# Optimization experiments

Hardware: AMD Instinct MI355X
Metric: run time of the kernel (lower is better)

## Reference

```python
import jax, jax.numpy as jnp
import numpy as np

TEMPERATURE = 0.07
EPS = 1e-07


def setup_inputs() -> dict:
    key = jax.random.key(0)
    kf, kl = jax.random.split(key)
    bsz, n_views, d = 4096, 2, 256
    feats = jax.random.normal(kf, (bsz, n_views, d), dtype=jnp.float32)
    # L2-normalize per view, as in standard SupCon pipelines
    feats = feats / jnp.linalg.norm(feats, axis=-1, keepdims=True)
    labels = jax.random.randint(kl, (bsz,), 0, 3, dtype=jnp.int64 if jax.config.jax_enable_x64 else jnp.int32)
    return {"features": feats, "labels": labels}


def reference(features, labels):
    bsz, n_views, d = features.shape
    n = bsz * n_views
    # torch.cat(torch.unbind(features, dim=1), dim=0): views stacked along batch
    contrast_feature = jnp.transpose(features, (1, 0, 2)).reshape(n, d)
    anchor_feature = contrast_feature  # contrast_mode == 'all'

    # label-equality mask with the module's 1e-7 offset, tiled over views
    mask_small = (labels[:, None] == labels[None, :]).astype(jnp.float32) + EPS
    mask = jnp.tile(mask_small, (n_views, n_views))  # [n, n]

    logits_mask = 1.0 - jnp.eye(n, dtype=jnp.float32)  # zero out self-contrast
    mask_pos = mask * logits_mask
    mask_neg = (1.0 - mask) * logits_mask

    similarity = jnp.exp(jnp.matmul(anchor_feature, contrast_feature.T) / TEMPERATURE)
    pos = jnp.sum(similarity * mask_pos, axis=1)
    neg = jnp.sum(similarity * mask_neg, axis=1)
    loss = -jnp.mean(jnp.log(pos / (pos + neg)))
    return loss
```

## Files before the change

kernel.cpp:

```cpp
#include <hip/hip_runtime.h>
#include <cstdint>

#define BSZ   4096
#define NTOT  8192
#define DIM   256
#define BT    128
#define BKE   128
#define NCB   (NTOT / BT)
#define NBLK  (NCB * (NCB + 1) / 2)
#define INV_T (1.0f/0.07f)

typedef __bf16 bf16x8 __attribute__((ext_vector_type(8)));
typedef float  f32x4  __attribute__((ext_vector_type(4)));

#define GLOAD_LDS16(gp, lp)                                                  \
  __builtin_amdgcn_global_load_lds(                                          \
      (const __attribute__((address_space(1))) void*)(gp),                   \
      (__attribute__((address_space(3))) void*)(lp), 16, 0, 0)

__device__ __forceinline__ unsigned short f2bf(float f) {
  unsigned int u = __float_as_uint(f);
  u = u + 0x7FFFu + ((u >> 16) & 1u);
  return (unsigned short)(u >> 16);
}

__global__ __launch_bounds__(256) void cvt_kernel(const float* __restrict__ F,
                                                  unsigned short* __restrict__ X,
                                                  float* __restrict__ gsum,
                                                  int* __restrict__ gcnt) {
  if (blockIdx.x == 0 && threadIdx.x == 0) { *gsum = 0.f; *gcnt = 0; }
  int t = blockIdx.x * 256 + threadIdx.x;
  int r = t >> 6;
  int k = (t & 63) << 2;
  const float4 v = *(const float4*)(F + (size_t)(r & (BSZ - 1)) * (2 * DIM)
                                      + (r >> 12) * DIM + k);
  ushort4 o = make_ushort4(f2bf(v.x), f2bf(v.y), f2bf(v.z), f2bf(v.w));
  *(ushort4*)(X + (size_t)r * DIM + k) = o;
}

__global__ __launch_bounds__(256) void supcon_kernel(
    const unsigned short* __restrict__ X, const int* __restrict__ lab,
    float* __restrict__ partTot, float* __restrict__ partEq) {
  __shared__ unsigned short lA[BT * BKE];
  __shared__ unsigned short lB[BT * BKE];

  const int tid  = threadIdx.x;
  const int lane = tid & 63;
  const int wave = tid >> 6;
  const int wr   = (wave >> 1) * 64;
  const int wc   = (wave & 1) * 64;
  const int l15  = lane & 15;
  const int quad = lane >> 4;

  const int b = blockIdx.x;
  const int c = (b & 7) * (NBLK / 8) + (b >> 3);
  int i, j;
  if (c < 1792) {
    const int spo = c >> 6;
    const int w   = c & 63;
    int g1 = 0, rem = spo;
    while (rem >= 7 - g1) { rem -= 7 - g1; ++g1; }
    const int g2 = g1 + 1 + rem;
    i = g1 * 8 + (w >> 3);
    j = g2 * 8 + (w & 7);
  } else {
    const int c2 = c - 1792;
    const int g  = c2 / 36;
    int w = c2 - g * 36;
    int a = 0;
    while (w >= 8 - a) { w -= 8 - a; ++a; }
    i = g * 8 + a;
    j = g * 8 + a + w;
  }
  const int RB = i * BT;
  const int CB = j * BT;

  int colIdx[4], colLab[4];
#pragma unroll
  for (int tc = 0; tc < 4; ++tc) {
    colIdx[tc] = CB + wc + tc * 16 + l15;
    colLab[tc] = lab[colIdx[tc] & (BSZ - 1)];
  }
  int rowLab[4][4];
#pragma unroll
  for (int tr = 0; tr < 4; ++tr)
#pragma unroll
    for (int reg = 0; reg < 4; ++reg)
      rowLab[tr][reg] = lab[(RB + wr + tr * 16 + quad * 4 + reg) & (BSZ - 1)];

  const int srow  = lane >> 4;
  const unsigned short* gA = X + (size_t)(RB + wave * 32 + srow) * DIM;
  const unsigned short* gB = X + (size_t)(CB + wave * 32 + srow) * DIM;

  f32x4 acc[4][4] = {};

  for (int kb = 0; kb < DIM; kb += BKE) {
    __syncthreads();
#pragma unroll
    for (int l = 0; l < 8; ++l) {
      const int chunk = (lane & 15) ^ ((l * 4 + srow) & 15);
      GLOAD_LDS16(gA + (size_t)(l * 4) * DIM + kb + chunk * 8,
                  lA + (wave * 32 + l * 4) * BKE);
      GLOAD_LDS16(gB + (size_t)(l * 4) * DIM + kb + chunk * 8,
                  lB + (wave * 32 + l * 4) * BKE);
    }
    __syncthreads();

#pragma unroll
    for (int sub = 0; sub < 4; ++sub) {
      bf16x8 aF[4], bF[4];
      const int slot = ((sub * 4 + quad) ^ l15) * 8;
#pragma unroll
      for (int t = 0; t < 4; ++t) {
        aF[t] = *(const bf16x8*)(lA + (wr + t * 16 + l15) * BKE + slot);
        bF[t] = *(const bf16x8*)(lB + (wc + t * 16 + l15) * BKE + slot);
      }
#pragma unroll
      for (int tr = 0; tr < 4; ++tr)
#pragma unroll
        for (int tc = 0; tc < 4; ++tc)
          acc[tr][tc] = __builtin_amdgcn_mfma_f32_16x16x32_bf16(
              aF[tr], bF[tc], acc[tr][tc], 0, 0, 0);
    }
  }

  if (i == j) {
#pragma unroll
    for (int tr = 0; tr < 4; ++tr)
#pragma unroll
      for (int tc = 0; tc < 4; ++tc)
#pragma unroll
        for (int reg = 0; reg < 4; ++reg) {
          const int row = RB + wr + tr * 16 + quad * 4 + reg;
          float e = __expf(acc[tr][tc][reg] * INV_T);
          acc[tr][tc][reg] = (colIdx[tc] == row) ? 0.f : e;
        }
  } else {
#pragma unroll
    for (int tr = 0; tr < 4; ++tr)
#pragma unroll
      for (int tc = 0; tc < 4; ++tc)
#pragma unroll
        for (int reg = 0; reg < 4; ++reg)
          acc[tr][tc][reg] = __expf(acc[tr][tc][reg] * INV_T);
  }

  __syncthreads();
  float* sbuf = (float*)lA;
#pragma unroll
  for (int tr = 0; tr < 4; ++tr) {
#pragma unroll
    for (int reg = 0; reg < 4; ++reg) {
      float tot = 0.f, eqs = 0.f;
#pragma unroll
      for (int tc = 0; tc < 4; ++tc) {
        const float e = acc[tr][tc][reg];
        tot += e;
        if (colLab[tc] == rowLab[tr][reg]) eqs += e;
      }
#pragma unroll
      for (int off = 1; off < 16; off <<= 1) {
        tot += __shfl_xor(tot, off, 64);
        eqs += __shfl_xor(eqs, off, 64);
      }
      if (l15 == 0) {
        const int rl_ = wr + tr * 16 + quad * 4 + reg;
        sbuf[(wave & 1) * 128 + rl_]       = tot;
        sbuf[256 + (wave & 1) * 128 + rl_] = eqs;
      }
    }
  }
  if (i != j) {
#pragma unroll
    for (int tc = 0; tc < 4; ++tc) {
      float tt = 0.f, te = 0.f;
#pragma unroll
      for (int tr = 0; tr < 4; ++tr)
#pragma unroll
        for (int reg = 0; reg < 4; ++reg) {
          const float e = acc[tr][tc][reg];
          tt += e;
          if (rowLab[tr][reg] == colLab[tc]) te += e;
        }
      tt += __shfl_xor(tt, 16, 64);  te += __shfl_xor(te, 16, 64);
      tt += __shfl_xor(tt, 32, 64);  te += __shfl_xor(te, 32, 64);
      if (quad == 0) {
        const int cl_ = wc + tc * 16 + l15;
        sbuf[512 + (wave >> 1) * 128 + cl_] = tt;
        sbuf[768 + (wave >> 1) * 128 + cl_] = te;
      }
    }
  }
  __syncthreads();

  if (tid < 128) {
    partTot[(size_t)j * NTOT + RB + tid] = sbuf[tid] + sbuf[128 + tid];
    partEq [(size_t)j * NTOT + RB + tid] = sbuf[256 + tid] + sbuf[384 + tid];
  } else if (i != j) {
    const int c2 = tid - 128;
    partTot[(size_t)i * NTOT + CB + c2] = sbuf[512 + c2] + sbuf[640 + c2];
    partEq [(size_t)i * NTOT + CB + c2] = sbuf[768 + c2] + sbuf[896 + c2];
  }
}

__global__ __launch_bounds__(128) void reduce_kernel(
    const float* __restrict__ partTot, const float* __restrict__ partEq,
    float* __restrict__ gsum, int* __restrict__ gcnt,
    unsigned int* __restrict__ out) {
  const int r = blockIdx.x * 128 + threadIdx.x;
  float tot = 0.f, eqs = 0.f;
#pragma unroll 8
  for (int cb = 0; cb < NCB; ++cb) {
    tot += partTot[(size_t)cb * NTOT + r];
    eqs += partEq [(size_t)cb * NTOT + r];
  }
  const float term = __logf((eqs + 1e-7f * tot) / tot);
  __shared__ float red[128];
  red[threadIdx.x] = term;
  __syncthreads();
  for (int step = 64; step > 0; step >>= 1) {
    if (threadIdx.x < step) red[threadIdx.x] += red[threadIdx.x + step];
    __syncthreads();
  }
  if (threadIdx.x == 0) {
    atomicAdd(gsum, red[0]);
    __threadfence();
    const int old = atomicAdd(gcnt, 1);
    if (old == (int)gridDim.x - 1) {
      __threadfence();
      const float total = atomicAdd(gsum, 0.0f);
      const float loss = -total / (float)NTOT;
      const unsigned short bb = f2bf(loss);
      out[0] = ((unsigned int)bb << 16) | (unsigned int)bb;
    }
  }
}

extern "C" void kernel_launch(void* const* d_in, const int* in_sizes, int n_in,
                              void* d_out, int out_size, void* d_ws, size_t ws_size,
                              hipStream_t stream) {
  (void)in_sizes; (void)n_in; (void)out_size; (void)ws_size;
  const float* feats = (const float*)d_in[0];
  const int*   labels = (const int*)d_in[1];

  char* ws = (char*)d_ws;
  unsigned short* X = (unsigned short*)ws;
  float* partTot = (float*)(ws + (size_t)NTOT * DIM * 2);
  float* partEq  = partTot + (size_t)NCB * NTOT;
  float* gsum    = partEq  + (size_t)NCB * NTOT;
  int*   gcnt    = (int*)(gsum + 1);

  cvt_kernel<<<NTOT * DIM / 4 / 256, 256, 0, stream>>>(feats, X, gsum, gcnt);
  supcon_kernel<<<NBLK, 256, 0, stream>>>(X, labels, partTot, partEq);
  reduce_kernel<<<NTOT / 128, 128, 0, stream>>>(partTot, partEq, gsum, gcnt,
                                                (unsigned int*)d_out);
}
```

Measured before the change: 115.0 us.

## Pre-swizzle features into MFMA fragment layout and load fragments directly from global

The conversion kernel now writes the bf16 features in a layout matching the MFMA 16x16x32 fragment order, so each lane's 8-element fragment is contiguous. The GEMM kernel drops the LDS staging, its swizzled global-to-LDS loads and the barriers, and reads A/B fragments straight from global/L2, with launch bounds raised to target 3 blocks per CU. This removes LDS traffic and synchronisation, but each wave now loads its own fragments and data sharing within a block depends on the cache, which raises global/L2 load traffic.

```diff
diff --git a/kernel.cpp b/kernel.cpp
--- a/kernel.cpp
+++ b/kernel.cpp
@@ -5,18 +5,12 @@
 #define NTOT  8192
 #define DIM   256
 #define BT    128
-#define BKE   128
 #define NCB   (NTOT / BT)
 #define NBLK  (NCB * (NCB + 1) / 2)
 #define INV_T (1.0f/0.07f)
 
 typedef __bf16 bf16x8 __attribute__((ext_vector_type(8)));
 typedef float  f32x4  __attribute__((ext_vector_type(4)));
-
-#define GLOAD_LDS16(gp, lp)                                                  \
-  __builtin_amdgcn_global_load_lds(                                          \
-      (const __attribute__((address_space(1))) void*)(gp),                   \
-      (__attribute__((address_space(3))) void*)(lp), 16, 0, 0)
 
 __device__ __forceinline__ unsigned short f2bf(float f) {
   unsigned int u = __float_as_uint(f);
@@ -24,25 +18,30 @@
   return (unsigned short)(u >> 16);
 }
 
+
 __global__ __launch_bounds__(256) void cvt_kernel(const float* __restrict__ F,
-                                                  unsigned short* __restrict__ X,
+                                                  unsigned short* __restrict__ Xf,
                                                   float* __restrict__ gsum,
                                                   int* __restrict__ gcnt) {
   if (blockIdx.x == 0 && threadIdx.x == 0) { *gsum = 0.f; *gcnt = 0; }
-  int t = blockIdx.x * 256 + threadIdx.x;
-  int r = t >> 6;
-  int k = (t & 63) << 2;
-  const float4 v = *(const float4*)(F + (size_t)(r & (BSZ - 1)) * (2 * DIM)
-                                      + (r >> 12) * DIM + k);
-  ushort4 o = make_ushort4(f2bf(v.x), f2bf(v.y), f2bf(v.z), f2bf(v.w));
-  *(ushort4*)(X + (size_t)r * DIM + k) = o;
-}
-
-__global__ __launch_bounds__(256) void supcon_kernel(
-    const unsigned short* __restrict__ X, const int* __restrict__ lab,
+  const int v = blockIdx.x * 256 + threadIdx.x;
+  const int T = v >> 9;
+  const int c = (v >> 4) & 31;
+  const int p = v & 15;
+  const int r = T * 16 + p;
+  const float* src = F + (size_t)(r & (BSZ - 1)) * (2 * DIM) + (r >> 12) * DIM + c * 8;
+  const float4 v0 = *(const float4*)src;
+  const float4 v1 = *(const float4*)(src + 4);
+  ushort4 o0 = make_ushort4(f2bf(v0.x), f2bf(v0.y), f2bf(v0.z), f2bf(v0.w));
+  ushort4 o1 = make_ushort4(f2bf(v1.x), f2bf(v1.y), f2bf(v1.z), f2bf(v1.w));
+  *(ushort4*)(Xf + (size_t)v * 8)     = o0;
+  *(ushort4*)(Xf + (size_t)v * 8 + 4) = o1;
+}
+
+__global__ __launch_bounds__(256, 3) void supcon_kernel(
+    const unsigned short* __restrict__ Xf, const int* __restrict__ lab,
     float* __restrict__ partTot, float* __restrict__ partEq) {
-  __shared__ unsigned short lA[BT * BKE];
-  __shared__ unsigned short lB[BT * BKE];
+  __shared__ float sbuf[1024];
 
   const int tid  = threadIdx.x;
   const int lane = tid & 63;
@@ -88,40 +87,27 @@
     for (int reg = 0; reg < 4; ++reg)
       rowLab[tr][reg] = lab[(RB + wr + tr * 16 + quad * 4 + reg) & (BSZ - 1)];
 
-  const int srow  = lane >> 4;
-  const unsigned short* gA = X + (size_t)(RB + wave * 32 + srow) * DIM;
-  const unsigned short* gB = X + (size_t)(CB + wave * 32 + srow) * DIM;
+  const int TA = (RB >> 4) + (wave >> 1) * 4;
+  const int TB = (CB >> 4) + (wave & 1) * 4;
+  const int lo = quad * 128 + l15 * 8;
 
   f32x4 acc[4][4] = {};
 
-  for (int kb = 0; kb < DIM; kb += BKE) {
-    __syncthreads();
-#pragma unroll
-    for (int l = 0; l < 8; ++l) {
-      const int chunk = (lane & 15) ^ ((l * 4 + srow) & 15);
-      GLOAD_LDS16(gA + (size_t)(l * 4) * DIM + kb + chunk * 8,
-                  lA + (wave * 32 + l * 4) * BKE);
-      GLOAD_LDS16(gB + (size_t)(l * 4) * DIM + kb + chunk * 8,
-                  lB + (wave * 32 + l * 4) * BKE);
-    }
-    __syncthreads();
-
-#pragma unroll
-    for (int sub = 0; sub < 4; ++sub) {
-      bf16x8 aF[4], bF[4];
-      const int slot = ((sub * 4 + quad) ^ l15) * 8;
-#pragma unroll
-      for (int t = 0; t < 4; ++t) {
-        aF[t] = *(const bf16x8*)(lA + (wr + t * 16 + l15) * BKE + slot);
-        bF[t] = *(const bf16x8*)(lB + (wc + t * 16 + l15) * BKE + slot);
-      }
-#pragma unroll
-      for (int tr = 0; tr < 4; ++tr)
-#pragma unroll
-        for (int tc = 0; tc < 4; ++tc)
-          acc[tr][tc] = __builtin_amdgcn_mfma_f32_16x16x32_bf16(
-              aF[tr], bF[tc], acc[tr][tc], 0, 0, 0);
-    }
+#pragma unroll
+  for (int kb = 0; kb < 8; ++kb) {
+    bf16x8 aF[4], bF[4];
+    const int ko = kb * 512 + lo;
+#pragma unroll
+    for (int t = 0; t < 4; ++t) {
+      aF[t] = *(const bf16x8*)(Xf + (size_t)(TA + t) * 4096 + ko);
+      bF[t] = *(const bf16x8*)(Xf + (size_t)(TB + t) * 4096 + ko);
+    }
+#pragma unroll
+    for (int tr = 0; tr < 4; ++tr)
+#pragma unroll
+      for (int tc = 0; tc < 4; ++tc)
+        acc[tr][tc] = __builtin_amdgcn_mfma_f32_16x16x32_bf16(
+            aF[tr], bF[tc], acc[tr][tc], 0, 0, 0);
   }
 
   if (i == j) {
@@ -145,8 +131,6 @@
           acc[tr][tc][reg] = __expf(acc[tr][tc][reg] * INV_T);
   }
 
-  __syncthreads();
-  float* sbuf = (float*)lA;
 #pragma unroll
   for (int tr = 0; tr < 4; ++tr) {
 #pragma unroll
@@ -244,14 +228,14 @@
   const int*   labels = (const int*)d_in[1];
 
   char* ws = (char*)d_ws;
-  unsigned short* X = (unsigned short*)ws;
+  unsigned short* Xf = (unsigned short*)ws;
   float* partTot = (float*)(ws + (size_t)NTOT * DIM * 2);
   float* partEq  = partTot + (size_t)NCB * NTOT;
   float* gsum    = partEq  + (size_t)NCB * NTOT;
   int*   gcnt    = (int*)(gsum + 1);
 
-  cvt_kernel<<<NTOT * DIM / 4 / 256, 256, 0, stream>>>(feats, X, gsum, gcnt);
-  supcon_kernel<<<NBLK, 256, 0, stream>>>(X, labels, partTot, partEq);
+  cvt_kernel<<<NTOT * DIM / 8 / 256, 256, 0, stream>>>(feats, Xf, gsum, gcnt);
+  supcon_kernel<<<NBLK, 256, 0, stream>>>(Xf, labels, partTot, partEq);
   reduce_kernel<<<NTOT / 128, 128, 0, stream>>>(partTot, partEq, gsum, gcnt,
                                                 (unsigned int*)d_out);
 }
```

After: 106.8 us. 7.1% less time.
